# Kernel tuning notes

Measured on AMD Instinct MI355X. Metric: run time of the kernel, lower is better.

The kernel has to match this reference:

```python
import jax, jax.numpy as jnp
import numpy as np

D_MODEL = 512
N = 2048
BS = 8


def setup_inputs() -> dict:
    key = jax.random.key(0)
    ks = jax.random.split(key, 5)
    inputs1 = jax.random.normal(ks[0], (BS, N, D_MODEL), dtype=jnp.float32)
    inputs2 = jax.random.normal(ks[1], (BS, N, D_MODEL), dtype=jnp.float32)
    # torch Linear weights: init.normal_(std=0.001), bias=0
    Wq = 0.001 * jax.random.normal(ks[2], (D_MODEL, D_MODEL), dtype=jnp.float32)
    Wk = 0.001 * jax.random.normal(ks[3], (D_MODEL, D_MODEL), dtype=jnp.float32)
    Wv = 0.001 * jax.random.normal(ks[4], (D_MODEL, D_MODEL), dtype=jnp.float32)
    bq = jnp.zeros((D_MODEL,), dtype=jnp.float32)
    bk = jnp.zeros((D_MODEL,), dtype=jnp.float32)
    bv = jnp.zeros((D_MODEL,), dtype=jnp.float32)
    # nn.Parameter(torch.ones((n, n)))
    position_biases = jnp.ones((N, N), dtype=jnp.float32)
    return {"inputs1": inputs1, "inputs2": inputs2, "Wq": Wq, "bq": bq,
            "Wk": Wk, "bk": bk, "Wv": Wv, "bv": bv,
            "position_biases": position_biases}


def reference(inputs1, inputs2, Wq, bq, Wk, bk, Wv, bv, position_biases):
    # torch Linear: y = x @ W.T + b
    q = inputs1 @ Wq.T + bq                     # [b, n, d]
    k = inputs1 @ Wk.T + bk                     # [b, s, d]
    v = inputs2 @ Wv.T + bv                     # [b, s, d]
    # exp(k[b,s,d] + bias[t,s]) = exp(bias)[t,s] * exp(k)[b,s,d] -> separable,
    # avoiding the original's (n, bs, n, dim) broadcast intermediate.
    expB = jnp.exp(position_biases)             # [t, s]
    ek = jnp.exp(k)                             # [b, s, d]
    num = jnp.einsum('ts,bsd->btd', expB, ek * v)
    den = jnp.einsum('ts,bsd->btd', expB, ek)
    return jax.nn.sigmoid(q) * (num / den)      # [b, n, d]
```

## Files before the change

### kernel.cpp

```cpp
#include <hip/hip_runtime.h>

typedef float  f32x4  __attribute__((ext_vector_type(4)));
typedef __bf16 bf16x8 __attribute__((ext_vector_type(8)));
typedef __bf16 bf16x4 __attribute__((ext_vector_type(4)));

#define D_MODEL 512
#define SEQ     2048
#define BATCH   8
#define ROWS    (BATCH * SEQ)

#define ASYNC_COPY16(dst_lds, src_glb)                                          \
  __builtin_amdgcn_global_load_lds(                                             \
      (const __attribute__((address_space(1))) void*)(src_glb),                 \
      (__attribute__((address_space(3))) void*)(dst_lds), 16, 0, 0)

__global__ void cvt_all_kernel(const float* __restrict__ x1,
                               const float* __restrict__ x2,
                               const float* __restrict__ posb,
                               const float* __restrict__ Wq,
                               const float* __restrict__ Wk,
                               const float* __restrict__ Wv,
                               __bf16* __restrict__ x1b, __bf16* __restrict__ x2b,
                               __bf16* __restrict__ expBb, __bf16* __restrict__ wb)
{
  const int blk = blockIdx.x;
  if (blk < 16384) {
    const float* in = (blk < 8192) ? x1 : x2;
    __bf16* out = (blk < 8192) ? x1b : x2b;
    const int i = (blk & 8191) * 256 + threadIdx.x;
    float4 v = ((const float4*)in)[i];
    bf16x4 o = { (__bf16)v.x, (__bf16)v.y, (__bf16)v.z, (__bf16)v.w };
    ((bf16x4*)out)[i] = o;
  } else if (blk < 20480) {
    const int i = (blk - 16384) * 256 + threadIdx.x;
    float4 v = ((const float4*)posb)[i];
    bf16x4 o = { (__bf16)__expf(v.x), (__bf16)__expf(v.y),
                 (__bf16)__expf(v.z), (__bf16)__expf(v.w) };
    ((bf16x4*)expBb)[i] = o;
  } else {
    const int i = (blk - 20480) * 256 + threadIdx.x;
    const int nW4 = D_MODEL * D_MODEL / 4;
    const float* src = (i < nW4) ? Wq : (i < 2 * nW4) ? Wk : Wv;
    const int ii = i - ((i < nW4) ? 0 : (i < 2 * nW4) ? nW4 : 2 * nW4);
    float4 v = ((const float4*)src)[ii];
    bf16x4 o = { (__bf16)v.x, (__bf16)v.y, (__bf16)v.z, (__bf16)v.w };
    ((bf16x4*)wb)[i] = o;
  }
}

#define TNT (D_MODEL / 64)

__global__ __launch_bounds__(512) void tri_gemm_kernel(
    const __bf16* __restrict__ x1b, const __bf16* __restrict__ x2b,
    const __bf16* __restrict__ wb,
    const float* __restrict__ bq, const float* __restrict__ bk,
    const float* __restrict__ bv,
    __bf16* __restrict__ sigq, __bf16* __restrict__ kT,
    __bf16* __restrict__ vT)
{
  extern __shared__ __align__(16) __bf16 smem[];

  const int K = D_MODEL;
  const int z = blockIdx.z;
  const int tid  = threadIdx.x;
  const int wave = tid >> 6;
  const int lane = tid & 63;
  const int quad = lane >> 4;
  const int l16  = lane & 15;
  const int wm   = (wave >> 2) * 128;
  const int wn   = (wave & 3) * 64;
  const int L0   = blockIdx.x * 256;
  const int F0   = blockIdx.y * 256;
  const int m0   = (z == 0) ? L0 : F0;
  const int n0   = (z == 0) ? F0 : L0;
  const int l8r  = lane >> 3;
  const int scol = ((lane & 7) ^ l8r) * 8;

  const __bf16* Ap = (z == 0) ? x1b
                   : (z == 1) ? (wb + (long long)D_MODEL * D_MODEL)
                              : (wb + 2LL * D_MODEL * D_MODEL);
  const __bf16* Bp = (z == 0) ? wb : (z == 1) ? x1b : x2b;

  const __bf16* gA = Ap + (long long)(m0 + wave * 8 + l8r) * K + scol;
  const __bf16* gB = Bp + (long long)(n0 + wave * 8 + l8r) * K + scol;
  __bf16* lA = smem +         (wave * 8) * 64;
  __bf16* lB = smem + 32768 + (wave * 8) * 64;

  f32x4 acc[8][4];
  #pragma unroll
  for (int i = 0; i < 8; ++i)
    #pragma unroll
    for (int j = 0; j < 4; ++j) acc[i][j] = (f32x4){0.f, 0.f, 0.f, 0.f};

  auto stage_pair = [&](int c, int k0, int i) {
    ASYNC_COPY16(lA + c * 16384 + i * 4096, gA + (long long)i * 64 * K + k0);
    ASYNC_COPY16(lB + c * 16384 + i * 4096, gB + (long long)i * 64 * K + k0);
  };

  #pragma unroll
  for (int i = 0; i < 4; ++i) stage_pair(0, 0, i);

  const int s0 = ((quad    ) ^ (l16 & 7)) * 8;
  const int s1 = ((quad + 4) ^ (l16 & 7)) * 8;

  for (int t = 0; t < TNT; ++t) {
    const int c = t & 1;
    asm volatile("s_waitcnt vmcnt(0)" ::: "memory");
    __builtin_amdgcn_s_barrier();
    __builtin_amdgcn_sched_barrier(0);

    const __bf16* Ac = smem +         c * 16384 + (wm + l16) * 64;
    const __bf16* Bc = smem + 32768 + c * 16384 + (wn + l16) * 64;
    const bool pf = (t + 1 < TNT);
    const int k1 = (t + 1) * 64;

    bf16x8 bfr[4][2];
    #pragma unroll
    for (int q = 0; q < 4; ++q) {
      if (q == 0) {
        #pragma unroll
        for (int j = 0; j < 4; ++j) {
          bfr[j][0] = *(const bf16x8*)&Bc[j * 1024 + s0];
          bfr[j][1] = *(const bf16x8*)&Bc[j * 1024 + s1];
        }
      }
      bf16x8 af[2][2];
      #pragma unroll
      for (int ii = 0; ii < 2; ++ii) {
        af[ii][0] = *(const bf16x8*)&Ac[(q * 2 + ii) * 1024 + s0];
        af[ii][1] = *(const bf16x8*)&Ac[(q * 2 + ii) * 1024 + s1];
      }
      if (pf) {
        if (q == 0) { stage_pair(c ^ 1, k1, 0); stage_pair(c ^ 1, k1, 1); }
        else if (q == 1) { stage_pair(c ^ 1, k1, 2); stage_pair(c ^ 1, k1, 3); }
      }
      __builtin_amdgcn_s_barrier();
      asm volatile("s_waitcnt lgkmcnt(0)" ::: "memory");
      __builtin_amdgcn_sched_barrier(0);
      __builtin_amdgcn_s_setprio(1);
      #pragma unroll
      for (int kk = 0; kk < 2; ++kk)
        #pragma unroll
        for (int ii = 0; ii < 2; ++ii)
          #pragma unroll
          for (int j = 0; j < 4; ++j)
            acc[q * 2 + ii][j] = __builtin_amdgcn_mfma_f32_16x16x32_bf16(
                af[ii][kk], bfr[j][kk], acc[q * 2 + ii][j], 0, 0, 0);
      __builtin_amdgcn_s_setprio(0);
      __builtin_amdgcn_s_barrier();
    }
  }

  if (z == 0) {
    #pragma unroll
    for (int j = 0; j < 4; ++j) {
      const int col = n0 + wn + j * 16 + l16;
      const float bvv = bq[col];
      #pragma unroll
      for (int i = 0; i < 8; ++i) {
        #pragma unroll
        for (int r = 0; r < 4; ++r) {
          const int row = m0 + wm + i * 16 + quad * 4 + r;
          float x = acc[i][j][r] + bvv;
          sigq[(long long)row * D_MODEL + col] =
              (__bf16)(1.f / (1.f + __expf(-x)));
        }
      }
    }
  } else {
    const float* bias = (z == 1) ? bk : bv;
    __bf16* outp = (z == 1) ? kT : vT;
    #pragma unroll
    for (int i = 0; i < 8; ++i) {
      #pragma unroll
      for (int r = 0; r < 4; ++r) {
        const int d = m0 + wm + i * 16 + quad * 4 + r;
        const float bvv = bias[d];
        #pragma unroll
        for (int j = 0; j < 4; ++j) {
          const int rr = n0 + wn + j * 16 + l16;
          outp[(long long)d * ROWS + rr] = (__bf16)(acc[i][j][r] + bvv);
        }
      }
    }
  }
}

__global__ __launch_bounds__(256) void combine_kernel(
    const __bf16* __restrict__ kT, const __bf16* __restrict__ vT,
    __bf16* __restrict__ ekvT)
{
  const int c = blockIdx.x * 256 + threadIdx.x;
  const int d   = c >> 11;
  const int off = (c & 2047) * 8;
  const int b = off >> 11;
  const int s = off & 2047;

  bf16x8 kk = *(const bf16x8*)(kT + (long long)d * ROWS + off);
  bf16x8 vv = *(const bf16x8*)(vT + (long long)d * ROWS + off);
  bf16x8 ek, ev;
  #pragma unroll
  for (int e = 0; e < 8; ++e) {
    float ekf = __expf((float)kk[e]);
    ek[e] = (__bf16)ekf;
    ev[e] = (__bf16)(ekf * (float)vv[e]);
  }
  const int gr = ((d >> 5) << 6) + (d & 31);
  __bf16* outp = ekvT + (long long)b * (2 * D_MODEL) * SEQ + s;
  *(bf16x8*)(outp + (long long)gr * SEQ)        = ev;
  *(bf16x8*)(outp + (long long)(gr + 32) * SEQ) = ek;
}

#define EBM 256
#define EBN 256
#define EBK 64
#define ENT (SEQ / EBK)

__global__ __launch_bounds__(512) void einsum_fused_kernel(
    const __bf16* __restrict__ A, const __bf16* __restrict__ BtAll,
    const __bf16* __restrict__ sigq, float* __restrict__ out)
{
  extern __shared__ __align__(16) __bf16 smem[];

  const int b = blockIdx.z;
  const __bf16* Bt = BtAll + (long long)b * (2 * D_MODEL) * SEQ;

  const int tid  = threadIdx.x;
  const int wave = tid >> 6;
  const int lane = tid & 63;
  const int quad = lane >> 4;
  const int l16  = lane & 15;
  const int wm   = (wave >> 2) * 128;
  const int wn   = (wave & 3) * 64;
  const int m0   = blockIdx.x * EBM;
  const int n0   = blockIdx.y * EBN;
  const int l8r  = lane >> 3;
  const int scol = ((lane & 7) ^ l8r) * 8;

  const __bf16* gA = A  + (long long)(m0 + wave * 8 + l8r) * SEQ + scol;
  const __bf16* gB = Bt + (long long)(n0 + wave * 8 + l8r) * SEQ + scol;
  __bf16* lA = smem +         (wave * 8) * 64;
  __bf16* lB = smem + 32768 + (wave * 8) * 64;

  f32x4 acc[8][4];
  #pragma unroll
  for (int i = 0; i < 8; ++i)
    #pragma unroll
    for (int j = 0; j < 4; ++j) acc[i][j] = (f32x4){0.f, 0.f, 0.f, 0.f};

  auto stage_pair = [&](int c, int k0, int i) {
    ASYNC_COPY16(lA + c * 16384 + i * 4096, gA + (long long)i * 64 * SEQ + k0);
    ASYNC_COPY16(lB + c * 16384 + i * 4096, gB + (long long)i * 64 * SEQ + k0);
  };

  #pragma unroll
  for (int i = 0; i < 4; ++i) stage_pair(0, 0, i);

  const int s0 = ((quad    ) ^ (l16 & 7)) * 8;
  const int s1 = ((quad + 4) ^ (l16 & 7)) * 8;

  for (int t = 0; t < ENT; ++t) {
    const int c = t & 1;
    asm volatile("s_waitcnt vmcnt(0)" ::: "memory");
    __builtin_amdgcn_s_barrier();
    __builtin_amdgcn_sched_barrier(0);

    const __bf16* Ac = smem +         c * 16384 + (wm + l16) * 64;
    const __bf16* Bc = smem + 32768 + c * 16384 + (wn + l16) * 64;
    const bool pf = (t + 1 < ENT);
    const int k1 = (t + 1) * EBK;

    bf16x8 bfr[4][2];
    #pragma unroll
    for (int q = 0; q < 4; ++q) {
      if (q == 0) {
        #pragma unroll
        for (int j = 0; j < 4; ++j) {
          bfr[j][0] = *(const bf16x8*)&Bc[j * 1024 + s0];
          bfr[j][1] = *(const bf16x8*)&Bc[j * 1024 + s1];
        }
      }
      bf16x8 af[2][2];
      #pragma unroll
      for (int ii = 0; ii < 2; ++ii) {
        af[ii][0] = *(const bf16x8*)&Ac[(q * 2 + ii) * 1024 + s0];
        af[ii][1] = *(const bf16x8*)&Ac[(q * 2 + ii) * 1024 + s1];
      }
      if (pf) {
        if (q == 0) { stage_pair(c ^ 1, k1, 0); stage_pair(c ^ 1, k1, 1); }
        else if (q == 1) { stage_pair(c ^ 1, k1, 2); stage_pair(c ^ 1, k1, 3); }
      }
      __builtin_amdgcn_s_barrier();
      asm volatile("s_waitcnt lgkmcnt(0)" ::: "memory");
      __builtin_amdgcn_sched_barrier(0);
      __builtin_amdgcn_s_setprio(1);
      #pragma unroll
      for (int kk = 0; kk < 2; ++kk)
        #pragma unroll
        for (int ii = 0; ii < 2; ++ii)
          #pragma unroll
          for (int j = 0; j < 4; ++j)
            acc[q * 2 + ii][j] = __builtin_amdgcn_mfma_f32_16x16x32_bf16(
                af[ii][kk], bfr[j][kk], acc[q * 2 + ii][j], 0, 0, 0);
      __builtin_amdgcn_s_setprio(0);
      __builtin_amdgcn_s_barrier();
    }
  }

  const int g = (n0 + wn) >> 6;
  #pragma unroll
  for (int j = 0; j < 2; ++j) {
    const int d = g * 32 + j * 16 + l16;
    #pragma unroll
    for (int i = 0; i < 8; ++i) {
      #pragma unroll
      for (int r = 0; r < 4; ++r) {
        const int row = m0 + wm + i * 16 + quad * 4 + r;
        const long long off = ((long long)b * SEQ + row) * D_MODEL + d;
        const float num = acc[i][j][r];
        const float den = acc[i][j + 2][r];
        out[off] = (float)sigq[off] * (num / den);
      }
    }
  }
}

extern "C" void kernel_launch(void* const* d_in, const int* in_sizes, int n_in,
                              void* d_out, int out_size, void* d_ws, size_t ws_size,
                              hipStream_t stream) {
  const float* inputs1 = (const float*)d_in[0];
  const float* inputs2 = (const float*)d_in[1];
  const float* Wq = (const float*)d_in[2];
  const float* bq = (const float*)d_in[3];
  const float* Wk = (const float*)d_in[4];
  const float* bk = (const float*)d_in[5];
  const float* Wv = (const float*)d_in[6];
  const float* bv = (const float*)d_in[7];
  const float* posb = (const float*)d_in[8];
  float* out = (float*)d_out;

  char* ws = (char*)d_ws;
  const long long szX  = (long long)ROWS * D_MODEL * 2;
  const long long szW  = (long long)D_MODEL * D_MODEL * 2;
  const long long szEB = (long long)SEQ * SEQ * 2;
  const long long szT  = (long long)BATCH * 2 * D_MODEL * SEQ * 2;
  __bf16* x1b   = (__bf16*)(ws);                 ws += szX;
  __bf16* x2b   = (__bf16*)(ws);                 ws += szX;
  __bf16* wb    = (__bf16*)(ws);                 ws += 3 * szW;
  __bf16* expBb = (__bf16*)(ws);                 ws += szEB;
  __bf16* sigq  = (__bf16*)(ws);                 ws += szX;
  __bf16* kT    = (__bf16*)(ws);                 ws += szX;
  __bf16* vT    = (__bf16*)(ws);                 ws += szX;
  __bf16* ekvT  = (__bf16*)(ws);                 ws += szT;

  static bool attr_done = false;
  if (!attr_done) {
    hipFuncSetAttribute((const void*)einsum_fused_kernel,
                        hipFuncAttributeMaxDynamicSharedMemorySize, 131072);
    hipFuncSetAttribute((const void*)tri_gemm_kernel,
                        hipFuncAttributeMaxDynamicSharedMemorySize, 131072);
    attr_done = true;
  }

  cvt_all_kernel<<<21248, 256, 0, stream>>>(inputs1, inputs2, posb,
                                            Wq, Wk, Wv,
                                            x1b, x2b, expBb, wb);

  {
    dim3 g(ROWS / 256, D_MODEL / 256, 3);
    tri_gemm_kernel<<<g, 512, 131072, stream>>>(x1b, x2b, wb, bq, bk, bv,
                                                sigq, kT, vT);
  }

  combine_kernel<<<(D_MODEL * ROWS / 8) / 256, 256, 0, stream>>>(kT, vT, ekvT);

  {
    dim3 g(SEQ / EBM, (2 * D_MODEL) / EBN, BATCH);
    einsum_fused_kernel<<<g, 512, 131072, stream>>>(expBb, ekvT, sigq, out);
  }
}
```

Measured before the change: 254.1 us.

## Fuse K/V projections with exp combine into one kernel, split Q GEMM

Replaces the three-way GEMM plus separate combine kernel with a Q-only GEMM and a fused K/V GEMM. The fused kernel computes K and V tiles for the same rows, applies bias, exp and the product in its epilogue, and writes the interleaved ekvT layout directly. This removes the kT/vT round trip through global memory and one kernel launch. Both GEMMs now use smaller 256x128 tiles with less LDS, which raises the number of blocks. The K/V kernel holds two accumulator sets per wave, which increases register pressure, and its ekvT stores are column-scattered 2-byte writes.

```diff
diff --git a/kernel.cpp b/kernel.cpp
--- a/kernel.cpp
+++ b/kernel.cpp
@@ -48,76 +48,68 @@
   }
 }
 
-#define TNT (D_MODEL / 64)
-
-__global__ __launch_bounds__(512) void tri_gemm_kernel(
-    const __bf16* __restrict__ x1b, const __bf16* __restrict__ x2b,
-    const __bf16* __restrict__ wb,
-    const float* __restrict__ bq, const float* __restrict__ bk,
-    const float* __restrict__ bv,
-    __bf16* __restrict__ sigq, __bf16* __restrict__ kT,
-    __bf16* __restrict__ vT)
+__global__ __launch_bounds__(512) void q_gemm_kernel(
+    const __bf16* __restrict__ x1b, const __bf16* __restrict__ wb,
+    const float* __restrict__ bq, __bf16* __restrict__ sigq)
 {
   extern __shared__ __align__(16) __bf16 smem[];
 
   const int K = D_MODEL;
-  const int z = blockIdx.z;
   const int tid  = threadIdx.x;
   const int wave = tid >> 6;
   const int lane = tid & 63;
   const int quad = lane >> 4;
   const int l16  = lane & 15;
-  const int wm   = (wave >> 2) * 128;
-  const int wn   = (wave & 3) * 64;
-  const int L0   = blockIdx.x * 256;
-  const int F0   = blockIdx.y * 256;
-  const int m0   = (z == 0) ? L0 : F0;
-  const int n0   = (z == 0) ? F0 : L0;
+  const int wm   = (wave >> 1) * 64;
+  const int wn   = (wave & 1) * 64;
+  const int m0   = blockIdx.x * 256;
+  const int n0   = blockIdx.y * 128;
   const int l8r  = lane >> 3;
   const int scol = ((lane & 7) ^ l8r) * 8;
 
-  const __bf16* Ap = (z == 0) ? x1b
-                   : (z == 1) ? (wb + (long long)D_MODEL * D_MODEL)
-                              : (wb + 2LL * D_MODEL * D_MODEL);
-  const __bf16* Bp = (z == 0) ? wb : (z == 1) ? x1b : x2b;
-
-  const __bf16* gA = Ap + (long long)(m0 + wave * 8 + l8r) * K + scol;
-  const __bf16* gB = Bp + (long long)(n0 + wave * 8 + l8r) * K + scol;
-  __bf16* lA = smem +         (wave * 8) * 64;
-  __bf16* lB = smem + 32768 + (wave * 8) * 64;
-
-  f32x4 acc[8][4];
-  #pragma unroll
-  for (int i = 0; i < 8; ++i)
+  const __bf16* ga[4]; const __bf16* gb[2];
+  #pragma unroll
+  for (int i = 0; i < 4; ++i)
+    ga[i] = x1b + (long long)(m0 + i * 64 + wave * 8 + l8r) * K + scol;
+  #pragma unroll
+  for (int i = 0; i < 2; ++i)
+    gb[i] = wb + (long long)(n0 + i * 64 + wave * 8 + l8r) * K + scol;
+
+  f32x4 acc[4][4];
+  #pragma unroll
+  for (int i = 0; i < 4; ++i)
     #pragma unroll
     for (int j = 0; j < 4; ++j) acc[i][j] = (f32x4){0.f, 0.f, 0.f, 0.f};
 
-  auto stage_pair = [&](int c, int k0, int i) {
-    ASYNC_COPY16(lA + c * 16384 + i * 4096, gA + (long long)i * 64 * K + k0);
-    ASYNC_COPY16(lB + c * 16384 + i * 4096, gB + (long long)i * 64 * K + k0);
+  auto stageA2 = [&](int c, int k0, int i0) {
+    ASYNC_COPY16(smem + c * 16384 + (i0 * 64 + wave * 8) * 64, ga[i0] + k0);
+    ASYNC_COPY16(smem + c * 16384 + ((i0 + 1) * 64 + wave * 8) * 64, ga[i0 + 1] + k0);
   };
-
-  #pragma unroll
-  for (int i = 0; i < 4; ++i) stage_pair(0, 0, i);
+  auto stageB1 = [&](int c, int k0, int i) {
+    ASYNC_COPY16(smem + 32768 + c * 8192 + (i * 64 + wave * 8) * 64, gb[i] + k0);
+  };
+
+  stageA2(0, 0, 0); stageA2(0, 0, 2);
+  stageB1(0, 0, 0); stageB1(0, 0, 1);
 
   const int s0 = ((quad    ) ^ (l16 & 7)) * 8;
   const int s1 = ((quad + 4) ^ (l16 & 7)) * 8;
 
-  for (int t = 0; t < TNT; ++t) {
+  for (int t = 0; t < 8; ++t) {
     const int c = t & 1;
     asm volatile("s_waitcnt vmcnt(0)" ::: "memory");
     __builtin_amdgcn_s_barrier();
     __builtin_amdgcn_sched_barrier(0);
 
     const __bf16* Ac = smem +         c * 16384 + (wm + l16) * 64;
-    const __bf16* Bc = smem + 32768 + c * 16384 + (wn + l16) * 64;
-    const bool pf = (t + 1 < TNT);
+    const __bf16* Bc = smem + 32768 + c * 8192  + (wn + l16) * 64;
+    const bool pf = (t + 1 < 8);
     const int k1 = (t + 1) * 64;
 
     bf16x8 bfr[4][2];
     #pragma unroll
-    for (int q = 0; q < 4; ++q) {
-      if (q == 0) {
+    for (int p = 0; p < 2; ++p) {
+      if (p == 0) {
         #pragma unroll
         for (int j = 0; j < 4; ++j) {
           bfr[j][0] = *(const bf16x8*)&Bc[j * 1024 + s0];
@@ -127,12 +119,12 @@
       bf16x8 af[2][2];
       #pragma unroll
       for (int ii = 0; ii < 2; ++ii) {
-        af[ii][0] = *(const bf16x8*)&Ac[(q * 2 + ii) * 1024 + s0];
-        af[ii][1] = *(const bf16x8*)&Ac[(q * 2 + ii) * 1024 + s1];
+        af[ii][0] = *(const bf16x8*)&Ac[(p * 2 + ii) * 1024 + s0];
+        af[ii][1] = *(const bf16x8*)&Ac[(p * 2 + ii) * 1024 + s1];
       }
       if (pf) {
-        if (q == 0) { stage_pair(c ^ 1, k1, 0); stage_pair(c ^ 1, k1, 1); }
-        else if (q == 1) { stage_pair(c ^ 1, k1, 2); stage_pair(c ^ 1, k1, 3); }
+        if (p == 0) { stageA2(c ^ 1, k1, 0); stageB1(c ^ 1, k1, 0); }
+        else        { stageA2(c ^ 1, k1, 2); stageB1(c ^ 1, k1, 1); }
       }
       __builtin_amdgcn_s_barrier();
       asm volatile("s_waitcnt lgkmcnt(0)" ::: "memory");
@@ -144,71 +136,163 @@
         for (int ii = 0; ii < 2; ++ii)
           #pragma unroll
           for (int j = 0; j < 4; ++j)
-            acc[q * 2 + ii][j] = __builtin_amdgcn_mfma_f32_16x16x32_bf16(
-                af[ii][kk], bfr[j][kk], acc[q * 2 + ii][j], 0, 0, 0);
+            acc[p * 2 + ii][j] = __builtin_amdgcn_mfma_f32_16x16x32_bf16(
+                af[ii][kk], bfr[j][kk], acc[p * 2 + ii][j], 0, 0, 0);
       __builtin_amdgcn_s_setprio(0);
       __builtin_amdgcn_s_barrier();
     }
   }
 
-  if (z == 0) {
-    #pragma unroll
-    for (int j = 0; j < 4; ++j) {
-      const int col = n0 + wn + j * 16 + l16;
-      const float bvv = bq[col];
-      #pragma unroll
-      for (int i = 0; i < 8; ++i) {
-        #pragma unroll
-        for (int r = 0; r < 4; ++r) {
-          const int row = m0 + wm + i * 16 + quad * 4 + r;
-          float x = acc[i][j][r] + bvv;
-          sigq[(long long)row * D_MODEL + col] =
-              (__bf16)(1.f / (1.f + __expf(-x)));
-        }
-      }
-    }
-  } else {
-    const float* bias = (z == 1) ? bk : bv;
-    __bf16* outp = (z == 1) ? kT : vT;
-    #pragma unroll
-    for (int i = 0; i < 8; ++i) {
+  #pragma unroll
+  for (int j = 0; j < 4; ++j) {
+    const int col = n0 + wn + j * 16 + l16;
+    const float bvv = bq[col];
+    #pragma unroll
+    for (int i = 0; i < 4; ++i) {
       #pragma unroll
       for (int r = 0; r < 4; ++r) {
-        const int d = m0 + wm + i * 16 + quad * 4 + r;
-        const float bvv = bias[d];
-        #pragma unroll
-        for (int j = 0; j < 4; ++j) {
-          const int rr = n0 + wn + j * 16 + l16;
-          outp[(long long)d * ROWS + rr] = (__bf16)(acc[i][j][r] + bvv);
-        }
+        const int row = m0 + wm + i * 16 + quad * 4 + r;
+        float x = acc[i][j][r] + bvv;
+        sigq[(long long)row * D_MODEL + col] = (__bf16)(1.f / (1.f + __expf(-x)));
       }
     }
   }
 }
 
-__global__ __launch_bounds__(256) void combine_kernel(
-    const __bf16* __restrict__ kT, const __bf16* __restrict__ vT,
+__global__ __launch_bounds__(512) void kv_fused_kernel(
+    const __bf16* __restrict__ x1b, const __bf16* __restrict__ x2b,
+    const __bf16* __restrict__ wb,
+    const float* __restrict__ bk, const float* __restrict__ bv,
     __bf16* __restrict__ ekvT)
 {
-  const int c = blockIdx.x * 256 + threadIdx.x;
-  const int d   = c >> 11;
-  const int off = (c & 2047) * 8;
-  const int b = off >> 11;
-  const int s = off & 2047;
-
-  bf16x8 kk = *(const bf16x8*)(kT + (long long)d * ROWS + off);
-  bf16x8 vv = *(const bf16x8*)(vT + (long long)d * ROWS + off);
-  bf16x8 ek, ev;
-  #pragma unroll
-  for (int e = 0; e < 8; ++e) {
-    float ekf = __expf((float)kk[e]);
-    ek[e] = (__bf16)ekf;
-    ev[e] = (__bf16)(ekf * (float)vv[e]);
-  }
-  const int gr = ((d >> 5) << 6) + (d & 31);
-  __bf16* outp = ekvT + (long long)b * (2 * D_MODEL) * SEQ + s;
-  *(bf16x8*)(outp + (long long)gr * SEQ)        = ev;
-  *(bf16x8*)(outp + (long long)(gr + 32) * SEQ) = ek;
+  extern __shared__ __align__(16) __bf16 smem[];
+
+  const int K = D_MODEL;
+  const int tid  = threadIdx.x;
+  const int wave = tid >> 6;
+  const int lane = tid & 63;
+  const int quad = lane >> 4;
+  const int l16  = lane & 15;
+  const int wm   = (wave >> 1) * 64;
+  const int wn   = (wave & 1) * 64;
+  const int F0   = blockIdx.y * 256;
+  const int L0   = blockIdx.x * 128;
+  const int l8r  = lane >> 3;
+  const int scol = ((lane & 7) ^ l8r) * 8;
+  const bool hi  = (scol >= 32);
+  const int sc   = scol & 31;
+
+  const __bf16* Wkb = wb + (long long)D_MODEL * D_MODEL;
+  const __bf16* Wvb = wb + 2LL * D_MODEL * D_MODEL;
+
+  const __bf16* gW[4]; const __bf16* gX[2];
+  #pragma unroll
+  for (int i = 0; i < 4; ++i)
+    gW[i] = (hi ? Wvb : Wkb) + (long long)(F0 + i * 64 + wave * 8 + l8r) * K + sc;
+  #pragma unroll
+  for (int i = 0; i < 2; ++i)
+    gX[i] = (hi ? x2b : x1b) + (long long)(L0 + i * 64 + wave * 8 + l8r) * K + sc;
+
+  f32x4 acck[4][4], accv[4][4];
+  #pragma unroll
+  for (int i = 0; i < 4; ++i)
+    #pragma unroll
+    for (int j = 0; j < 4; ++j) {
+      acck[i][j] = (f32x4){0.f, 0.f, 0.f, 0.f};
+      accv[i][j] = (f32x4){0.f, 0.f, 0.f, 0.f};
+    }
+
+  auto stageW = [&](int c, int k0) {
+    #pragma unroll
+    for (int i = 0; i < 4; ++i)
+      ASYNC_COPY16(smem + c * 16384 + (i * 64 + wave * 8) * 64, gW[i] + k0);
+  };
+  auto stageX = [&](int c, int k0) {
+    #pragma unroll
+    for (int i = 0; i < 2; ++i)
+      ASYNC_COPY16(smem + 32768 + c * 8192 + (i * 64 + wave * 8) * 64, gX[i] + k0);
+  };
+
+  stageW(0, 0); stageX(0, 0);
+
+  const int s0 = ((quad    ) ^ (l16 & 7)) * 8;
+  const int s1 = ((quad + 4) ^ (l16 & 7)) * 8;
+
+  for (int s = 0; s < 16; ++s) {
+    const int c = s & 1;
+    asm volatile("s_waitcnt vmcnt(0)" ::: "memory");
+    __builtin_amdgcn_s_barrier();
+    __builtin_amdgcn_sched_barrier(0);
+
+    const __bf16* Wc = smem +         c * 16384 + (wm + l16) * 64;
+    const __bf16* Xc = smem + 32768 + c * 8192  + (wn + l16) * 64;
+    const bool pf = (s + 1 < 16);
+    const int k1 = (s + 1) * 32;
+
+    {
+      bf16x8 af[4], bfr[4];
+      #pragma unroll
+      for (int i = 0; i < 4; ++i) af[i]  = *(const bf16x8*)&Wc[i * 1024 + s0];
+      #pragma unroll
+      for (int j = 0; j < 4; ++j) bfr[j] = *(const bf16x8*)&Xc[j * 1024 + s0];
+      if (pf) stageW(c ^ 1, k1);
+      __builtin_amdgcn_s_barrier();
+      asm volatile("s_waitcnt lgkmcnt(0)" ::: "memory");
+      __builtin_amdgcn_sched_barrier(0);
+      __builtin_amdgcn_s_setprio(1);
+      #pragma unroll
+      for (int i = 0; i < 4; ++i)
+        #pragma unroll
+        for (int j = 0; j < 4; ++j)
+          acck[i][j] = __builtin_amdgcn_mfma_f32_16x16x32_bf16(
+              af[i], bfr[j], acck[i][j], 0, 0, 0);
+      __builtin_amdgcn_s_setprio(0);
+      __builtin_amdgcn_s_barrier();
+    }
+    {
+      bf16x8 af[4], bfr[4];
+      #pragma unroll
+      for (int i = 0; i < 4; ++i) af[i]  = *(const bf16x8*)&Wc[i * 1024 + s1];
+      #pragma unroll
+      for (int j = 0; j < 4; ++j) bfr[j] = *(const bf16x8*)&Xc[j * 1024 + s1];
+      if (pf) stageX(c ^ 1, k1);
+      __builtin_amdgcn_s_barrier();
+      asm volatile("s_waitcnt lgkmcnt(0)" ::: "memory");
+      __builtin_amdgcn_sched_barrier(0);
+      __builtin_amdgcn_s_setprio(1);
+      #pragma unroll
+      for (int i = 0; i < 4; ++i)
+        #pragma unroll
+        for (int j = 0; j < 4; ++j)
+          accv[i][j] = __builtin_amdgcn_mfma_f32_16x16x32_bf16(
+              af[i], bfr[j], accv[i][j], 0, 0, 0);
+      __builtin_amdgcn_s_setprio(0);
+      __builtin_amdgcn_s_barrier();
+    }
+  }
+
+  const int b   = L0 >> 11;
+  const int sb  = L0 & 2047;
+  __bf16* outb = ekvT + (long long)b * (2 * D_MODEL) * SEQ + sb;
+  #pragma unroll
+  for (int i = 0; i < 4; ++i) {
+    #pragma unroll
+    for (int r = 0; r < 4; ++r) {
+      const int d = F0 + wm + i * 16 + quad * 4 + r;
+      const float bkd = bk[d];
+      const float bvd = bv[d];
+      const int gr = ((d >> 5) << 6) + (d & 31);
+      #pragma unroll
+      for (int j = 0; j < 4; ++j) {
+        const int ss = wn + j * 16 + l16;
+        const float kkv = acck[i][j][r] + bkd;
+        const float vvv = accv[i][j][r] + bvd;
+        const float ekf = __expf(kkv);
+        outb[(long long)gr * SEQ + ss]        = (__bf16)(ekf * vvv);
+        outb[(long long)(gr + 32) * SEQ + ss] = (__bf16)ekf;
+      }
+    }
+  }
 }
 
 #define EBM 256
@@ -349,16 +433,16 @@
   __bf16* wb    = (__bf16*)(ws);                 ws += 3 * szW;
   __bf16* expBb = (__bf16*)(ws);                 ws += szEB;
   __bf16* sigq  = (__bf16*)(ws);                 ws += szX;
-  __bf16* kT    = (__bf16*)(ws);                 ws += szX;
-  __bf16* vT    = (__bf16*)(ws);                 ws += szX;
   __bf16* ekvT  = (__bf16*)(ws);                 ws += szT;
 
   static bool attr_done = false;
   if (!attr_done) {
     hipFuncSetAttribute((const void*)einsum_fused_kernel,
                         hipFuncAttributeMaxDynamicSharedMemorySize, 131072);
-    hipFuncSetAttribute((const void*)tri_gemm_kernel,
-                        hipFuncAttributeMaxDynamicSharedMemorySize, 131072);
+    hipFuncSetAttribute((const void*)q_gemm_kernel,
+                        hipFuncAttributeMaxDynamicSharedMemorySize, 98304);
+    hipFuncSetAttribute((const void*)kv_fused_kernel,
+                        hipFuncAttributeMaxDynamicSharedMemorySize, 98304);
     attr_done = true;
   }
 
@@ -367,12 +451,14 @@
                                             x1b, x2b, expBb, wb);
 
   {
-    dim3 g(ROWS / 256, D_MODEL / 256, 3);
-    tri_gemm_kernel<<<g, 512, 131072, stream>>>(x1b, x2b, wb, bq, bk, bv,
-                                                sigq, kT, vT);
-  }
-
-  combine_kernel<<<(D_MODEL * ROWS / 8) / 256, 256, 0, stream>>>(kT, vT, ekvT);
+    dim3 g(ROWS / 256, D_MODEL / 128);
+    q_gemm_kernel<<<g, 512, 98304, stream>>>(x1b, wb, bq, sigq);
+  }
+
+  {
+    dim3 g(ROWS / 128, D_MODEL / 256);
+    kv_fused_kernel<<<g, 512, 98304, stream>>>(x1b, x2b, wb, bk, bv, ekvT);
+  }
 
   {
     dim3 g(SEQ / EBM, (2 * D_MODEL) / EBN, BATCH);
```

Result: faster. 243.8 us (-4.0%).
